# Kernel tuning notes

Hardware: AMD Instinct MI355X
Metric: run time of the kernel (lower is better)

## Reference

```python
import jax, jax.numpy as jnp
import numpy as np
from jax import lax
from functools import partial

NPOINT = 2048
RADIUS = 1.0
NSAMPLE = 32


def _fps(xyz, npoint):
    # Farthest point sampling, sequential as in the classic CUDA kernel.
    # xyz: (N, 3) -> (npoint,) int32 indices; starts at index 0.
    N = xyz.shape[0]
    init_d = jnp.full((N,), jnp.inf, dtype=xyz.dtype)

    def step(carry, _):
        dists, last = carry
        delta = xyz - xyz[last]                      # (N, 3)
        nd = jnp.sum(delta * delta, axis=-1)         # (N,)
        dists = jnp.minimum(dists, nd)
        nxt = jnp.argmax(dists).astype(jnp.int32)
        return (dists, nxt), last

    (_, _), idxs = lax.scan(step, (init_d, jnp.int32(0)), None, length=npoint)
    return idxs


def _ball_query(radius, nsample, xyz, new_xyz):
    # xyz: (N, 3), new_xyz: (S, 3) -> (S, nsample) int32.
    # Take the first nsample points (in original order) within radius of each
    # centroid; pad with the first found index (centroid itself always hits).
    N = xyz.shape[0]
    d2 = (jnp.sum(new_xyz * new_xyz, -1, keepdims=True)
          + jnp.sum(xyz * xyz, -1)[None, :]
          - 2.0 * new_xyz @ xyz.T)                   # (S, N)
    mask = d2 < radius * radius
    key = jnp.where(mask, jnp.arange(N, dtype=jnp.int32), jnp.int32(N))  # (S, N)
    neg_topk, _ = lax.top_k(-key, nsample)           # nsample smallest keys
    idx = -neg_topk                                  # (S, nsample), ascending
    first = idx[:, :1]
    return jnp.where(idx == N, first, idx)


def setup_inputs() -> dict:
    key = jax.random.key(0)
    inputs = jax.random.normal(key, (4, 8192, 16), dtype=jnp.float32)
    return {"inputs": inputs}


def reference(inputs):
    xyz = inputs[..., :3]                            # (B, N, 3)
    points = inputs[..., 3:]                         # (B, N, C)

    fps_idx = jax.vmap(lambda p: _fps(p, NPOINT))(xyz)          # (B, S)
    new_xyz = jnp.take_along_axis(xyz, fps_idx[..., None], axis=1)  # (B, S, 3)

    idx = jax.vmap(partial(_ball_query, RADIUS, NSAMPLE))(xyz, new_xyz)  # (B, S, K)

    gather = jax.vmap(lambda p, i: p[i])             # (N, C), (S, K) -> (S, K, C)
    grouped_xyz = gather(xyz, idx) - new_xyz[:, :, None, :]      # (B, S, K, 3)
    grouped_points = gather(points, idx)                         # (B, S, K, C)
    new_points = jnp.concatenate([grouped_xyz, grouped_points], axis=-1)
    return new_xyz, new_points, idx, grouped_xyz
```

## Files before the change

kernel.cpp:

```cpp
#include <hip/hip_runtime.h>

#pragma clang fp contract(off)

#define NPOINT 2048
#define NSAMPLE 32
#define NPTS 8192
#define NB 4
#define CH 16
#define FPS_THREADS 512
#define PTS_PER_THREAD (NPTS / FPS_THREADS)
#define PAIRS (PTS_PER_THREAD / 2)
#define FPS_WAVES (FPS_THREADS / 64)

typedef unsigned long long u64;
typedef float v2f __attribute__((ext_vector_type(2)));

#define OFF_NEWXYZ 0
#define OFF_NEWPTS (NB * NPOINT * 3)
#define OFF_IDX (OFF_NEWPTS + NB * NPOINT * NSAMPLE * CH)
#define OFF_GXYZ (OFF_IDX + NB * NPOINT * NSAMPLE)

template <int CTRL>
__device__ __forceinline__ float dpp_fmax(float v) {
  int o = __builtin_amdgcn_update_dpp(0, __float_as_int(v), CTRL, 0xf, 0xf, true);
  return fmaxf(v, __int_as_float(o));
}

__global__ __launch_bounds__(FPS_THREADS)
__attribute__((amdgpu_waves_per_eu(2))) void fps_kernel(
    const float* __restrict__ in, float* __restrict__ out) {
  __shared__ float4 lpxyz[NPTS];
  __shared__ float newb[NPOINT * 3];
  __shared__ alignas(16) u64 slots[2][FPS_WAVES];

  const int b = blockIdx.x;
  const int tid = threadIdx.x;
  const int lane = tid & 63;
  const int wv = tid >> 6;
  const float* base = in + (size_t)b * NPTS * CH;

  v2f pxv[PAIRS], pyv[PAIRS], pzv[PAIRS], dv[PAIRS];
#pragma unroll
  for (int jp = 0; jp < PAIRS; ++jp) {
    int p0 = tid * PTS_PER_THREAD + 2 * jp;
    float4 r0 = *reinterpret_cast<const float4*>(base + (size_t)p0 * CH);
    float4 r1 = *reinterpret_cast<const float4*>(base + (size_t)(p0 + 1) * CH);
    pxv[jp] = (v2f){r0.x, r1.x};
    pyv[jp] = (v2f){r0.y, r1.y};
    pzv[jp] = (v2f){r0.z, r1.z};
    lpxyz[p0] = r0;
    lpxyz[p0 + 1] = r1;
    dv[jp] = (v2f){__builtin_inff(), __builtin_inff()};
  }
  if (tid < FPS_WAVES)
    slots[0][tid] = (tid == 0) ? (((u64)0x7f800000u << 32) | 8191u) : 0ull;

  for (int it = 0; it < NPOINT; ++it) {
    __syncthreads();
    const ulonglong2* sp =
        reinterpret_cast<const ulonglong2*>(&slots[it & 1][0]);
    const ulonglong2 s01 = sp[0];
    const ulonglong2 s23 = sp[1];
    const ulonglong2 s45 = sp[2];
    const ulonglong2 s67 = sp[3];
    u64 ka = (s01.y > s01.x) ? s01.y : s01.x;
    u64 kb = (s23.y > s23.x) ? s23.y : s23.x;
    u64 kc = (s45.y > s45.x) ? s45.y : s45.x;
    u64 kd = (s67.y > s67.x) ? s67.y : s67.x;
    ka = (kb > ka) ? kb : ka;
    kc = (kd > kc) ? kd : kc;
    const u64 k = (kc > ka) ? kc : ka;
    const int gi = 8191 - (int)(unsigned)k;
    const float4 g = lpxyz[gi];
    const float gx = g.x, gy = g.y, gz = g.z;
    if (tid == 0) {
      newb[it * 3 + 0] = gx;
      newb[it * 3 + 1] = gy;
      newb[it * 3 + 2] = gz;
    }
    float bestv = -1.0f;
    float bestx = -1.0f;
    int bestjp = 0;
#pragma unroll
    for (int jp = 0; jp < PAIRS; ++jp) {
      v2f dx = pxv[jp] - gx;
      v2f dy = pyv[jp] - gy;
      v2f dz = pzv[jp] - gz;
      v2f nd = (dx * dx + dy * dy) + dz * dz;
      v2f dn = {fminf(dv[jp].x, nd.x), fminf(dv[jp].y, nd.y)};
      dv[jp] = dn;
      float pm = fmaxf(dn.x, dn.y);
      bool t = pm > bestv;
      bestjp = t ? jp : bestjp;
      bestx = t ? dn.x : bestx;
      bestv = fmaxf(bestv, pm);
    }
    const int bestj = 2 * bestjp + ((bestx == bestv) ? 0 : 1);
    const unsigned besti = (unsigned)(tid * PTS_PER_THREAD + bestj);
    float wm = bestv;
    wm = dpp_fmax<0x111>(wm);
    wm = dpp_fmax<0x112>(wm);
    wm = dpp_fmax<0x114>(wm);
    wm = dpp_fmax<0x118>(wm);
    wm = dpp_fmax<0x142>(wm);
    wm = dpp_fmax<0x143>(wm);
    const float swm =
        __int_as_float(__builtin_amdgcn_readlane(__float_as_int(wm), 63));
    const u64 wbal = __ballot(bestv == swm);
    const int wl = (int)__builtin_ctzll(wbal);
    if (lane == wl) {
      slots[(it + 1) & 1][wv] =
          ((u64)__float_as_uint(bestv) << 32) | (8191u - besti);
    }
  }
  __syncthreads();
  float* ob = out + OFF_NEWXYZ + (size_t)b * NPOINT * 3;
  for (int i = tid; i < NPOINT * 3; i += FPS_THREADS) ob[i] = newb[i];
}

__device__ __forceinline__ void write_slot(float* __restrict__ out,
                                           const float* __restrict__ base,
                                           int b, int qi, int s, int p,
                                           float4 r0, float qx, float qy,
                                           float qz) {
  float dx = __fsub_rn(r0.x, qx);
  float dy = __fsub_rn(r0.y, qy);
  float dz = __fsub_rn(r0.z, qz);
  size_t qs = (size_t)b * NPOINT + qi;
  out[OFF_IDX + qs * NSAMPLE + s] = (float)p;
  float* g = out + OFF_GXYZ + (qs * NSAMPLE + s) * 3;
  g[0] = dx;
  g[1] = dy;
  g[2] = dz;
  const float* row = base + (size_t)p * CH;
  float4 r1 = *reinterpret_cast<const float4*>(row + 4);
  float4 r2 = *reinterpret_cast<const float4*>(row + 8);
  float4 r3 = *reinterpret_cast<const float4*>(row + 12);
  float* np_ = out + OFF_NEWPTS + (qs * NSAMPLE + s) * CH;
  *reinterpret_cast<float4*>(np_ + 0) = make_float4(dx, dy, dz, r0.w);
  *reinterpret_cast<float4*>(np_ + 4) = r1;
  *reinterpret_cast<float4*>(np_ + 8) = r2;
  *reinterpret_cast<float4*>(np_ + 12) = r3;
}

__global__ __launch_bounds__(256) void ballq_kernel(
    const float* __restrict__ in, float* __restrict__ out) {
  const int lane = threadIdx.x & 63;
  const int qid = blockIdx.x * 4 + (threadIdx.x >> 6);
  const int b = qid >> 11;
  const int qi = qid & 2047;
  const float* base = in + (size_t)b * NPTS * CH;
  const float* q = out + OFF_NEWXYZ + ((size_t)b * NPOINT + qi) * 3;
  float qx = q[0], qy = q[1], qz = q[2];
  float qn = __fadd_rn(__fadd_rn(__fmul_rn(qx, qx), __fmul_rn(qy, qy)),
                       __fmul_rn(qz, qz));

  int cnt = 0;
  int first = 0;
  bool have_first = false;
  for (int chunk = 0; chunk < NPTS / 64 && cnt < NSAMPLE; ++chunk) {
    int p = chunk * 64 + lane;
    float4 r0 = *reinterpret_cast<const float4*>(base + (size_t)p * CH);
    float pn =
        __fadd_rn(__fadd_rn(__fmul_rn(r0.x, r0.x), __fmul_rn(r0.y, r0.y)),
                  __fmul_rn(r0.z, r0.z));
    float dot =
        __fadd_rn(__fadd_rn(__fmul_rn(qx, r0.x), __fmul_rn(qy, r0.y)),
                  __fmul_rn(qz, r0.z));
    float d2 = __fsub_rn(__fadd_rn(qn, pn), __fmul_rn(2.0f, dot));
    bool in_r = d2 < 1.0f;
    unsigned long long mask = __ballot(in_r);
    if (!have_first && mask) {
      first = chunk * 64 + __builtin_ctzll(mask);
      have_first = true;
    }
    int pos = cnt + __popcll(mask & ((1ull << lane) - 1ull));
    if (in_r && pos < NSAMPLE) write_slot(out, base, b, qi, pos, p, r0, qx, qy, qz);
    cnt += __popcll(mask);
  }
  if (cnt < NSAMPLE) {
    int s = cnt + lane;
    if (s < NSAMPLE) {
      float4 r0 = *reinterpret_cast<const float4*>(base + (size_t)first * CH);
      write_slot(out, base, b, qi, s, first, r0, qx, qy, qz);
    }
  }
}

extern "C" void kernel_launch(void* const* d_in, const int* in_sizes, int n_in,
                              void* d_out, int out_size, void* d_ws,
                              size_t ws_size, hipStream_t stream) {
  (void)in_sizes;
  (void)n_in;
  (void)out_size;
  (void)d_ws;
  (void)ws_size;
  const float* in = (const float*)d_in[0];
  float* out = (float*)d_out;
  fps_kernel<<<NB, FPS_THREADS, 0, stream>>>(in, out);
  ballq_kernel<<<(NB * NPOINT) / 4, 256, 0, stream>>>(in, out);
}
```

Measured before the change: 1.845 ms.

## Replace per-iteration FPS barrier with tagged LDS spin-wait flags

The farthest-point-sampling loop no longer calls __syncthreads each iteration. Each wave publishes its candidate into a double-buffered LDS slot, with the iteration number encoded in the index word and written with a release store. Readers spin with relaxed atomic loads until all eight slots carry the current tag. The aim is to cut block-wide barrier latency on the serial 2048-step critical path. The change also simplifies the running-max update and skips the distance work on the final iteration, at the cost of spin-polling overhead and reliance on correct memory ordering between waves.

```diff
diff --git a/kernel.cpp b/kernel.cpp
--- a/kernel.cpp
+++ b/kernel.cpp
@@ -31,7 +31,7 @@
     const float* __restrict__ in, float* __restrict__ out) {
   __shared__ float4 lpxyz[NPTS];
   __shared__ float newb[NPOINT * 3];
-  __shared__ alignas(16) u64 slots[2][FPS_WAVES];
+  __shared__ alignas(16) unsigned slotw[2][FPS_WAVES][2];
 
   const int b = blockIdx.x;
   const int tid = threadIdx.x;
@@ -52,25 +52,43 @@
     lpxyz[p0 + 1] = r1;
     dv[jp] = (v2f){__builtin_inff(), __builtin_inff()};
   }
-  if (tid < FPS_WAVES)
-    slots[0][tid] = (tid == 0) ? (((u64)0x7f800000u << 32) | 8191u) : 0ull;
+  if (tid < FPS_WAVES) {
+    slotw[0][tid][0] = (tid == 0) ? 8191u : 0u;
+    slotw[0][tid][1] = (tid == 0) ? 0x7f800000u : 0u;
+    slotw[1][tid][0] = 0u;
+    slotw[1][tid][1] = 0u;
+  }
+  __syncthreads();
 
   for (int it = 0; it < NPOINT; ++it) {
-    __syncthreads();
-    const ulonglong2* sp =
-        reinterpret_cast<const ulonglong2*>(&slots[it & 1][0]);
-    const ulonglong2 s01 = sp[0];
-    const ulonglong2 s23 = sp[1];
-    const ulonglong2 s45 = sp[2];
-    const ulonglong2 s67 = sp[3];
-    u64 ka = (s01.y > s01.x) ? s01.y : s01.x;
-    u64 kb = (s23.y > s23.x) ? s23.y : s23.x;
-    u64 kc = (s45.y > s45.x) ? s45.y : s45.x;
-    u64 kd = (s67.y > s67.x) ? s67.y : s67.x;
+    const int par = it & 1;
+    u64* sp = reinterpret_cast<u64*>(&slotw[par][0][0]);
+    const unsigned tagbase = (unsigned)it << 13;
+    u64 k0, k1, k2, k3, k4, k5, k6, k7;
+    for (;;) {
+      k0 = __hip_atomic_load(&sp[0], __ATOMIC_RELAXED, __HIP_MEMORY_SCOPE_WORKGROUP);
+      k1 = __hip_atomic_load(&sp[1], __ATOMIC_RELAXED, __HIP_MEMORY_SCOPE_WORKGROUP);
+      k2 = __hip_atomic_load(&sp[2], __ATOMIC_RELAXED, __HIP_MEMORY_SCOPE_WORKGROUP);
+      k3 = __hip_atomic_load(&sp[3], __ATOMIC_RELAXED, __HIP_MEMORY_SCOPE_WORKGROUP);
+      k4 = __hip_atomic_load(&sp[4], __ATOMIC_RELAXED, __HIP_MEMORY_SCOPE_WORKGROUP);
+      k5 = __hip_atomic_load(&sp[5], __ATOMIC_RELAXED, __HIP_MEMORY_SCOPE_WORKGROUP);
+      k6 = __hip_atomic_load(&sp[6], __ATOMIC_RELAXED, __HIP_MEMORY_SCOPE_WORKGROUP);
+      k7 = __hip_atomic_load(&sp[7], __ATOMIC_RELAXED, __HIP_MEMORY_SCOPE_WORKGROUP);
+      unsigned d = ((unsigned)k0 - tagbase) | ((unsigned)k1 - tagbase) |
+                   ((unsigned)k2 - tagbase) | ((unsigned)k3 - tagbase) |
+                   ((unsigned)k4 - tagbase) | ((unsigned)k5 - tagbase) |
+                   ((unsigned)k6 - tagbase) | ((unsigned)k7 - tagbase);
+      if (d < 8192u) break;
+      __builtin_amdgcn_s_sleep(1);
+    }
+    u64 ka = (k1 > k0) ? k1 : k0;
+    u64 kb = (k3 > k2) ? k3 : k2;
+    u64 kc = (k5 > k4) ? k5 : k4;
+    u64 kd = (k7 > k6) ? k7 : k6;
     ka = (kb > ka) ? kb : ka;
     kc = (kd > kc) ? kd : kc;
     const u64 k = (kc > ka) ? kc : ka;
-    const int gi = 8191 - (int)(unsigned)k;
+    const int gi = 8191 - (int)((unsigned)k & 8191u);
     const float4 g = lpxyz[gi];
     const float gx = g.x, gy = g.y, gz = g.z;
     if (tid == 0) {
@@ -78,6 +96,7 @@
       newb[it * 3 + 1] = gy;
       newb[it * 3 + 2] = gz;
     }
+    if (it == NPOINT - 1) break;
     float bestv = -1.0f;
     float bestx = -1.0f;
     int bestjp = 0;
@@ -89,11 +108,11 @@
       v2f nd = (dx * dx + dy * dy) + dz * dz;
       v2f dn = {fminf(dv[jp].x, nd.x), fminf(dv[jp].y, nd.y)};
       dv[jp] = dn;
-      float pm = fmaxf(dn.x, dn.y);
-      bool t = pm > bestv;
+      float nb = fmaxf(fmaxf(dn.x, dn.y), bestv);
+      bool t = nb > bestv;
       bestjp = t ? jp : bestjp;
       bestx = t ? dn.x : bestx;
-      bestv = fmaxf(bestv, pm);
+      bestv = nb;
     }
     const int bestj = 2 * bestjp + ((bestx == bestv) ? 0 : 1);
     const unsigned besti = (unsigned)(tid * PTS_PER_THREAD + bestj);
@@ -109,8 +128,11 @@
     const u64 wbal = __ballot(bestv == swm);
     const int wl = (int)__builtin_ctzll(wbal);
     if (lane == wl) {
-      slots[(it + 1) & 1][wv] =
-          ((u64)__float_as_uint(bestv) << 32) | (8191u - besti);
+      __hip_atomic_store(&slotw[par ^ 1][wv][1], __float_as_uint(bestv),
+                         __ATOMIC_RELAXED, __HIP_MEMORY_SCOPE_WORKGROUP);
+      __hip_atomic_store(&slotw[par ^ 1][wv][0],
+                         ((unsigned)(it + 1) << 13) | (8191u - besti),
+                         __ATOMIC_RELEASE, __HIP_MEMORY_SCOPE_WORKGROUP);
     }
   }
   __syncthreads();
```

Result: slower. 1.983 ms (+7.5%).
